# Performance work log

Measured on AMD Instinct MI355X. Metric: run time of the kernel, lower is better.

The kernel has to match this reference:

```python
import jax, jax.numpy as jnp
import numpy as np

MIN_NORM = 1e-15
BALL_EPS = 1e-5  # keep points strictly inside the unit ball (c = 1)


def _artanh(x):
    return jnp.arctanh(jnp.clip(x, -1.0 + BALL_EPS, 1.0 - BALL_EPS))


def expmap0(u):
    # Poincare ball exp map at the origin, c = 1
    n = jnp.clip(jnp.linalg.norm(u, axis=-1, keepdims=True), MIN_NORM)
    return jnp.tanh(n) * u / n


def mobius_matvec(M, x):
    # Mobius matrix-vector product applied to every row of x: [N, D] -> [N, D]
    x_n = jnp.clip(jnp.linalg.norm(x, axis=-1, keepdims=True), MIN_NORM)
    Mx = x @ M.T
    Mx_n = jnp.clip(jnp.linalg.norm(Mx, axis=-1, keepdims=True), MIN_NORM)
    return jnp.tanh(Mx_n / x_n * _artanh(x_n)) * Mx / Mx_n


def pairwise_sqdist(x):
    # sqdist(x_i, x_j) for all pairs via mobius_add(-x_i, x_j); x: [N, D] -> [N, N]
    u = -x[:, None, :]          # [N, 1, D]
    v = x[None, :, :]           # [1, N, D]
    xy = jnp.sum(u * v, axis=-1, keepdims=True)   # [N, N, 1]
    x2 = jnp.sum(u * u, axis=-1, keepdims=True)
    y2 = jnp.sum(v * v, axis=-1, keepdims=True)
    num = (1.0 + 2.0 * xy + y2) * u + (1.0 - x2) * v   # [N, N, D]
    den = jnp.clip(1.0 + 2.0 * xy + x2 * y2, MIN_NORM)
    ma_n = jnp.linalg.norm(num / den, axis=-1)          # [N, N]
    d = 2.0 * _artanh(ma_n)
    return d * d


def setup_inputs() -> dict:
    key = jax.random.key(0)
    k1, k2, k3 = jax.random.split(key, 3)
    N, D, L = 512, 256, 2
    H_euc = jax.random.normal(k1, (N, D), dtype=jnp.float32)
    att_W = jax.random.normal(k2, (L, D, D), dtype=jnp.float32) / np.sqrt(D)
    A = jax.random.randint(k3, (N, N), 0, 2).astype(bool)
    return {"H_euc": H_euc, "att_W": att_W, "A": A}


def reference(H_euc, att_W, A):
    H = expmap0(H_euc)                      # [N, D] on the Poincare ball
    L = att_W.shape[0]
    for l in range(L):
        Wh = mobius_matvec(att_W[l], H)     # one mobius matvec per node (hoisted out of the i,j loop)
        scores = pairwise_sqdist(Wh)        # [N, N] hyperbolic squared distances
        scores = jnp.where(A, scores, -10000.0)
        att = jax.nn.softmax(scores, axis=1)
        att = jnp.where(A, att, 0.0)
        H = att @ H                         # [N, D]
    return H
```

## Files before the change

### kernel.cpp

```cpp
#include <hip/hip_runtime.h>
#include <math.h>

#define NN 512
#define DD 256

__device__ __forceinline__ void wred_sum2(double& a, double& b){
  #pragma unroll
  for (int o = 32; o > 0; o >>= 1){
    a += __shfl_down(a, o);
    b += __shfl_down(b, o);
  }
}
__device__ void bred_sum2(double& a, double& b){
  __shared__ double sa[4], sb[4]; __shared__ double ra, rb;
  int lane = threadIdx.x & 63, w = threadIdx.x >> 6;
  wred_sum2(a, b);
  __syncthreads();
  if (lane == 0){ sa[w] = a; sb[w] = b; }
  __syncthreads();
  if (threadIdx.x == 0){
    ra = (sa[0] + sa[1]) + (sa[2] + sa[3]);
    rb = (sb[0] + sb[1]) + (sb[2] + sb[3]);
  }
  __syncthreads();
  a = ra; b = rb;
}

__device__ __forceinline__ double artanh_clip(double x){
  const double lim = 1.0 - 1e-5;
  if (x >  lim) x =  lim;
  if (x < -lim) x = -lim;
  return 0.5 * log((1.0 + x) / (1.0 - x));
}

__global__ __launch_bounds__(256) void matvec0_k(
    const float* __restrict__ Hin, const float* __restrict__ W,
    const float* __restrict__ W1, float* __restrict__ W1T,
    float* __restrict__ Hf, float* __restrict__ Wh, float* __restrict__ WhT,
    double* __restrict__ r2){
  __shared__ float h0s[DD], h1s[DD];
  __shared__ float tile[64][65];
  int b = blockIdx.x, t = threadIdx.x;
  int i0 = 2 * b, i1 = i0 + 1;
  float u0 = Hin[i0 * DD + t], u1 = Hin[i1 * DD + t];
  double n0 = (double)u0 * (double)u0, n1 = (double)u1 * (double)u1;
  bred_sum2(n0, n1);
  n0 = sqrt(n0); if (n0 < 1e-15) n0 = 1e-15;
  n1 = sqrt(n1); if (n1 < 1e-15) n1 = 1e-15;
  double t0 = tanh(n0), t1 = tanh(n1);
  float h0 = (float)(t0 / n0 * (double)u0);
  float h1 = (float)(t1 / n1 * (double)u1);
  Hf[i0 * DD + t] = h0; Hf[i1 * DD + t] = h1;
  double xn0 = t0 < 1e-15 ? 1e-15 : t0;
  double xn1 = t1 < 1e-15 ? 1e-15 : t1;
  h0s[t] = h0; h1s[t] = h1;
  __syncthreads();
  const float4* Wt = (const float4*)(W + t * DD);
  const float4* r0 = (const float4*)h0s;
  const float4* r1 = (const float4*)h1s;
  float4 A0 = {0,0,0,0}, A1 = {0,0,0,0};
  #pragma unroll 8
  for (int k = 0; k < DD / 4; k++){
    float4 w = Wt[k], x0 = r0[k], x1 = r1[k];
    A0.x = fmaf(x0.x, w.x, A0.x); A0.y = fmaf(x0.y, w.y, A0.y);
    A0.z = fmaf(x0.z, w.z, A0.z); A0.w = fmaf(x0.w, w.w, A0.w);
    A1.x = fmaf(x1.x, w.x, A1.x); A1.y = fmaf(x1.y, w.y, A1.y);
    A1.z = fmaf(x1.z, w.z, A1.z); A1.w = fmaf(x1.w, w.w, A1.w);
  }
  float mx0 = (A0.x + A0.y) + (A0.z + A0.w);
  float mx1 = (A1.x + A1.y) + (A1.z + A1.w);
  double m0 = (double)mx0 * (double)mx0, m1 = (double)mx1 * (double)mx1;
  bred_sum2(m0, m1);
  double mn0 = sqrt(m0); if (mn0 < 1e-15) mn0 = 1e-15;
  double mn1 = sqrt(m1); if (mn1 < 1e-15) mn1 = 1e-15;
  double th0 = tanh(mn0 / xn0 * artanh_clip(xn0));
  double th1 = tanh(mn1 / xn1 * artanh_clip(xn1));
  float w0 = (float)(mx0 * (th0 / mn0));
  float w1 = (float)(mx1 * (th1 / mn1));
  Wh[i0 * DD + t] = w0;  Wh[i1 * DD + t] = w1;
  WhT[t * NN + i0] = w0; WhT[t * NN + i1] = w1;
  if (t == 0){ r2[i0] = th0 * th0; r2[i1] = th1 * th1; }

  if (b < 16){
    int tr = b >> 2, tc = b & 3;
    int tx = t & 63, ty4 = t >> 6;
    #pragma unroll
    for (int yy = 0; yy < 64; yy += 4)
      tile[yy + ty4][tx] = W1[(tr * 64 + yy + ty4) * DD + tc * 64 + tx];
    __syncthreads();
    #pragma unroll
    for (int yy = 0; yy < 64; yy += 4)
      W1T[(tc * 64 + yy + ty4) * DD + tr * 64 + tx] = tile[tx][yy + ty4];
  }
}

template<bool LAST>
__global__ __launch_bounds__(512) void fused_k(
    const float* __restrict__ Wh, const float* __restrict__ WhT,
    const double* __restrict__ r2, const int* __restrict__ A,
    const float* __restrict__ H, const float* __restrict__ WT2,
    float* __restrict__ Hn, float* __restrict__ Whn,
    float* __restrict__ WhTn, double* __restrict__ r2n){
  int b = blockIdx.x, tid = threadIdx.x;
  int i0 = 2 * b;
  __shared__ float xs[2 * DD];
  __shared__ float a_s[2][NN];
  __shared__ float4 parts[1024];
  __shared__ double ssum[8];
  __shared__ float hn_s[2][DD];
  __shared__ double hnorm2[2];

  xs[tid] = Wh[i0 * DD + tid];
  __syncthreads();

  {
    int ks = tid >> 7, jq = tid & 127;
    const float4* WT4 = (const float4*)WhT;
    const float4* x04 = (const float4*)xs;
    const float4* x14 = (const float4*)(xs + DD);
    float4 p0 = {0,0,0,0}, p1 = {0,0,0,0};
    int kq0 = ks * 16;
    #pragma unroll 4
    for (int kk = 0; kk < 16; kk++){
      float4 xa = x04[kq0 + kk], xb = x14[kq0 + kk];
      const float4* wp = WT4 + (kq0 + kk) * 4 * 128 + jq;
      float4 w0 = wp[0], w1 = wp[128], w2 = wp[256], w3 = wp[384];
      p0.x = fmaf(xa.x, w0.x, p0.x); p0.y = fmaf(xa.x, w0.y, p0.y);
      p0.z = fmaf(xa.x, w0.z, p0.z); p0.w = fmaf(xa.x, w0.w, p0.w);
      p0.x = fmaf(xa.y, w1.x, p0.x); p0.y = fmaf(xa.y, w1.y, p0.y);
      p0.z = fmaf(xa.y, w1.z, p0.z); p0.w = fmaf(xa.y, w1.w, p0.w);
      p0.x = fmaf(xa.z, w2.x, p0.x); p0.y = fmaf(xa.z, w2.y, p0.y);
      p0.z = fmaf(xa.z, w2.z, p0.z); p0.w = fmaf(xa.z, w2.w, p0.w);
      p0.x = fmaf(xa.w, w3.x, p0.x); p0.y = fmaf(xa.w, w3.y, p0.y);
      p0.z = fmaf(xa.w, w3.z, p0.z); p0.w = fmaf(xa.w, w3.w, p0.w);
      p1.x = fmaf(xb.x, w0.x, p1.x); p1.y = fmaf(xb.x, w0.y, p1.y);
      p1.z = fmaf(xb.x, w0.z, p1.z); p1.w = fmaf(xb.x, w0.w, p1.w);
      p1.x = fmaf(xb.y, w1.x, p1.x); p1.y = fmaf(xb.y, w1.y, p1.y);
      p1.z = fmaf(xb.y, w1.z, p1.z); p1.w = fmaf(xb.y, w1.w, p1.w);
      p1.x = fmaf(xb.z, w2.x, p1.x); p1.y = fmaf(xb.z, w2.y, p1.y);
      p1.z = fmaf(xb.z, w2.z, p1.z); p1.w = fmaf(xb.z, w2.w, p1.w);
      p1.x = fmaf(xb.w, w3.x, p1.x); p1.y = fmaf(xb.w, w3.y, p1.y);
      p1.z = fmaf(xb.w, w3.z, p1.z); p1.w = fmaf(xb.w, w3.w, p1.w);
    }
    parts[(ks * 128 + jq) * 2 + 0] = p0;
    parts[(ks * 128 + jq) * 2 + 1] = p1;
  }
  __syncthreads();

  int sgC = tid >> 6, qC = tid & 63;
  const float4* H4 = (const float4*)H;
  float4 hpre[8];
  #pragma unroll
  for (int jj = 0; jj < 8; jj++) hpre[jj] = H4[(sgC * 64 + jj) * 64 + qC];

  int r = tid >> 8, j2 = tid & 255;
  int i = i0 + r;
  double X2 = r2[i];
  const float* pf = (const float*)parts;
  auto dsum = [&](int j) -> double {
    int base = (((j >> 2) * 2 + r) << 2) + (j & 3);
    return ((double)pf[base] + (double)pf[base + 1024])
         + ((double)pf[base + 2048] + (double)pf[base + 3072]);
  };
  double d0 = dsum(j2), d1 = dsum(j2 + 256);

  auto score = [&](double dot, double Y2, int jj) -> double {
    if (i == jj) return 0.0;
    double xy = -dot;
    double a  = 1.0 + 2.0 * xy + Y2;
    double bb = 1.0 - X2;
    double den = 1.0 + 2.0 * xy + X2 * Y2;
    if (den < 1e-15) den = 1e-15;
    double nn = a * a * X2 + 2.0 * a * bb * xy + bb * bb * Y2;
    if (nn < 0.0) nn = 0.0;
    double s = sqrt(nn);
    double smax = den * (1.0 - 1e-5);
    if (s > smax) s = smax;
    double d = log((den + s) / (den - s));
    return d * d;
  };

  double Y0 = r2[j2], Y1 = r2[j2 + 256];
  int m0 = A[i * NN + j2], m1 = A[i * NN + j2 + 256];
  double e0 = 0.0, e1 = 0.0;
  if (m0) e0 = exp(score(d0, Y0, j2) - 150.0);
  if (m1) e1 = exp(score(d1, Y1, j2 + 256) - 150.0);

  double part = e0 + e1;
  #pragma unroll
  for (int o = 32; o > 0; o >>= 1) part += __shfl_down(part, o);
  int w = tid >> 6, lane = tid & 63;
  if (lane == 0) ssum[w] = part;
  __syncthreads();
  int base4 = r * 4;
  double sum = (ssum[base4] + ssum[base4 + 1]) + (ssum[base4 + 2] + ssum[base4 + 3]);
  double inv = 1.0 / sum;
  a_s[r][j2]       = m0 ? (float)(e0 * inv) : 0.f;
  a_s[r][j2 + 256] = m1 ? (float)(e1 * inv) : 0.f;
  __syncthreads();

  {
    float4 c0 = {0,0,0,0}, c1 = {0,0,0,0};
    int jb = sgC * 64;
    #pragma unroll
    for (int jj = 0; jj < 8; jj++){
      int j = jb + jj;
      float a0 = a_s[0][j], a1 = a_s[1][j];
      float4 h = hpre[jj];
      c0.x = fmaf(a0, h.x, c0.x); c0.y = fmaf(a0, h.y, c0.y);
      c0.z = fmaf(a0, h.z, c0.z); c0.w = fmaf(a0, h.w, c0.w);
      c1.x = fmaf(a1, h.x, c1.x); c1.y = fmaf(a1, h.y, c1.y);
      c1.z = fmaf(a1, h.z, c1.z); c1.w = fmaf(a1, h.w, c1.w);
    }
    #pragma unroll 8
    for (int jj = 8; jj < 64; jj++){
      int j = jb + jj;
      float a0 = a_s[0][j], a1 = a_s[1][j];
      float4 h = H4[j * 64 + qC];
      c0.x = fmaf(a0, h.x, c0.x); c0.y = fmaf(a0, h.y, c0.y);
      c0.z = fmaf(a0, h.z, c0.z); c0.w = fmaf(a0, h.w, c0.w);
      c1.x = fmaf(a1, h.x, c1.x); c1.y = fmaf(a1, h.y, c1.y);
      c1.z = fmaf(a1, h.z, c1.z); c1.w = fmaf(a1, h.w, c1.w);
    }
    parts[sgC * 64 + qC]       = c0;
    parts[512 + sgC * 64 + qC] = c1;
  }
  __syncthreads();
  if (tid < 128){
    int rr = tid >> 6, qq = tid & 63;
    float4 p[8];
    #pragma unroll
    for (int s8 = 0; s8 < 8; s8++) p[s8] = parts[rr * 512 + s8 * 64 + qq];
    float4 o;
    o.x = ((p[0].x + p[1].x) + (p[2].x + p[3].x)) + ((p[4].x + p[5].x) + (p[6].x + p[7].x));
    o.y = ((p[0].y + p[1].y) + (p[2].y + p[3].y)) + ((p[4].y + p[5].y) + (p[6].y + p[7].y));
    o.z = ((p[0].z + p[1].z) + (p[2].z + p[3].z)) + ((p[4].z + p[5].z) + (p[6].z + p[7].z));
    o.w = ((p[0].w + p[1].w) + (p[2].w + p[3].w)) + ((p[4].w + p[5].w) + (p[6].w + p[7].w));
    ((float4*)(Hn + (i0 + rr) * DD))[qq] = o;
    if (!LAST){
      ((float4*)hn_s[rr])[qq] = o;
      double s = (double)o.x * o.x + (double)o.y * o.y
               + (double)o.z * o.z + (double)o.w * o.w;
      #pragma unroll
      for (int off = 32; off > 0; off >>= 1) s += __shfl_down(s, off);
      if (qq == 0) hnorm2[rr] = s;
    }
  }
  if (LAST) return;
  __syncthreads();

  {
    int ks2 = tid >> 6, dq = tid & 63;
    const float4* WT4b = (const float4*)WT2;
    const float* h0 = hn_s[0]; const float* h1 = hn_s[1];
    float4 p0 = {0,0,0,0}, p1 = {0,0,0,0};
    int k0 = ks2 * 32;
    #pragma unroll 8
    for (int kk = 0; kk < 32; kk++){
      int k = k0 + kk;
      float4 wv = WT4b[k * 64 + dq];
      float a0v = h0[k], a1v = h1[k];
      p0.x = fmaf(a0v, wv.x, p0.x); p0.y = fmaf(a0v, wv.y, p0.y);
      p0.z = fmaf(a0v, wv.z, p0.z); p0.w = fmaf(a0v, wv.w, p0.w);
      p1.x = fmaf(a1v, wv.x, p1.x); p1.y = fmaf(a1v, wv.y, p1.y);
      p1.z = fmaf(a1v, wv.z, p1.z); p1.w = fmaf(a1v, wv.w, p1.w);
    }
    parts[(ks2 * 64 + dq) * 2 + 0] = p0;
    parts[(ks2 * 64 + dq) * 2 + 1] = p1;
  }
  __syncthreads();
  {
    int rr = tid >> 8, d = tid & 255;
    const float* pf2 = (const float*)parts;
    int base = ((d >> 2) * 2 + rr) * 4 + (d & 3);
    float q0 = pf2[base]        + pf2[base + 512];
    float q1 = pf2[base + 1024] + pf2[base + 1536];
    float q2 = pf2[base + 2048] + pf2[base + 2560];
    float q3 = pf2[base + 3072] + pf2[base + 3584];
    float mx = (q0 + q1) + (q2 + q3);
    double m2 = (double)mx * (double)mx;
    #pragma unroll
    for (int o = 32; o > 0; o >>= 1) m2 += __shfl_down(m2, o);
    int w2 = tid >> 6, lane2 = tid & 63;
    if (lane2 == 0) ssum[w2] = m2;
    __syncthreads();
    int b4 = rr * 4;
    double m2sum = (ssum[b4] + ssum[b4 + 1]) + (ssum[b4 + 2] + ssum[b4 + 3]);
    double mn = sqrt(m2sum); if (mn < 1e-15) mn = 1e-15;
    double xn = sqrt(hnorm2[rr]); if (xn < 1e-15) xn = 1e-15;
    double th = tanh(mn / xn * artanh_clip(xn));
    float wv = (float)((double)mx * (th / mn));
    int irow = i0 + rr;
    Whn[irow * DD + d] = wv;
    WhTn[d * NN + irow] = wv;
    if (d == 0) r2n[irow] = th * th;
  }
}

extern "C" void kernel_launch(void* const* d_in, const int* in_sizes, int n_in,
                              void* d_out, int out_size, void* d_ws, size_t ws_size,
                              hipStream_t stream){
  const float* H_euc = (const float*)d_in[0];
  const float* W     = (const float*)d_in[1];
  const int*   A     = (const int*)d_in[2];
  float* out = (float*)d_out;

  float* Hf   = (float*)d_ws;
  float* Hn   = Hf   + NN * DD;
  float* Wh   = Hn   + NN * DD;
  float* WhT  = Wh   + NN * DD;
  float* Whb  = WhT  + NN * DD;
  float* WhTb = Whb  + NN * DD;
  float* W1T  = WhTb + NN * DD;
  double* r2  = (double*)(W1T + DD * DD);
  double* r2b = r2 + NN;

  matvec0_k<<<NN / 2, DD, 0, stream>>>(H_euc, W, W + DD * DD, W1T, Hf, Wh, WhT, r2);
  fused_k<false><<<NN / 2, 2 * DD, 0, stream>>>(Wh, WhT, r2, A, Hf, W1T, Hn, Whb, WhTb, r2b);
  fused_k<true> <<<NN / 2, 2 * DD, 0, stream>>>(Whb, WhTb, r2b, A, Hn, nullptr, out, nullptr, nullptr, nullptr);
}
```

Baseline: 52.92 us.

## Process four rows per block in fused kernel and pre-transpose both weight matrices

The fused attention kernel now handles four query rows per 1024-thread block instead of two. Each loaded WhT, H and W element is reused across four rows, and partial sums are reduced through shared memory in two halves. A separate transpose kernel now produces transposed copies of both layer weights, so the first matvec reads coalesced W0T columns with a split-K reduction instead of strided per-thread rows. The cost is an extra kernel launch, only 128 blocks (fewer than the number of CUs), and higher register and LDS pressure per block.

```diff
diff --git a/kernel.cpp b/kernel.cpp
--- a/kernel.cpp
+++ b/kernel.cpp
@@ -3,6 +3,14 @@
 
 #define NN 512
 #define DD 256
+
+#define FMA4(P, S, V) \
+  P.x = fmaf(S, (V).x, P.x); P.y = fmaf(S, (V).y, P.y); \
+  P.z = fmaf(S, (V).z, P.z); P.w = fmaf(S, (V).w, P.w);
+
+__device__ __forceinline__ float4 f4add(float4 a, float4 b){
+  return make_float4(a.x + b.x, a.y + b.y, a.z + b.z, a.w + b.w);
+}
 
 __device__ __forceinline__ void wred_sum2(double& a, double& b){
   #pragma unroll
@@ -33,15 +41,32 @@
   return 0.5 * log((1.0 + x) / (1.0 - x));
 }
 
+__global__ __launch_bounds__(256) void transpose_k(const float* __restrict__ W,
+                                                   float* __restrict__ W0T,
+                                                   float* __restrict__ W1T){
+  __shared__ float tile[64][65];
+  int b = blockIdx.x, t = threadIdx.x;
+  const float* src = (b < 16) ? W : (W + DD * DD);
+  float* dst = (b < 16) ? W0T : W1T;
+  int tb = b & 15, tr = tb >> 2, tc = tb & 3;
+  int tx = t & 63, ty4 = t >> 6;
+  #pragma unroll
+  for (int yy = 0; yy < 64; yy += 4)
+    tile[yy + ty4][tx] = src[(tr * 64 + yy + ty4) * DD + tc * 64 + tx];
+  __syncthreads();
+  #pragma unroll
+  for (int yy = 0; yy < 64; yy += 4)
+    dst[(tc * 64 + yy + ty4) * DD + tr * 64 + tx] = tile[tx][yy + ty4];
+}
+
 __global__ __launch_bounds__(256) void matvec0_k(
-    const float* __restrict__ Hin, const float* __restrict__ W,
-    const float* __restrict__ W1, float* __restrict__ W1T,
+    const float* __restrict__ Hin, const float* __restrict__ W0T,
     float* __restrict__ Hf, float* __restrict__ Wh, float* __restrict__ WhT,
     double* __restrict__ r2){
-  __shared__ float h0s[DD], h1s[DD];
-  __shared__ float tile[64][65];
   int b = blockIdx.x, t = threadIdx.x;
   int i0 = 2 * b, i1 = i0 + 1;
+  __shared__ float h0s[DD], h1s[DD];
+  __shared__ float4 mp[512];
   float u0 = Hin[i0 * DD + t], u1 = Hin[i1 * DD + t];
   double n0 = (double)u0 * (double)u0, n1 = (double)u1 * (double)u1;
   bred_sum2(n0, n1);
@@ -55,60 +80,55 @@
   double xn1 = t1 < 1e-15 ? 1e-15 : t1;
   h0s[t] = h0; h1s[t] = h1;
   __syncthreads();
-  const float4* Wt = (const float4*)(W + t * DD);
-  const float4* r0 = (const float4*)h0s;
-  const float4* r1 = (const float4*)h1s;
-  float4 A0 = {0,0,0,0}, A1 = {0,0,0,0};
-  #pragma unroll 8
-  for (int k = 0; k < DD / 4; k++){
-    float4 w = Wt[k], x0 = r0[k], x1 = r1[k];
-    A0.x = fmaf(x0.x, w.x, A0.x); A0.y = fmaf(x0.y, w.y, A0.y);
-    A0.z = fmaf(x0.z, w.z, A0.z); A0.w = fmaf(x0.w, w.w, A0.w);
-    A1.x = fmaf(x1.x, w.x, A1.x); A1.y = fmaf(x1.y, w.y, A1.y);
-    A1.z = fmaf(x1.z, w.z, A1.z); A1.w = fmaf(x1.w, w.w, A1.w);
-  }
-  float mx0 = (A0.x + A0.y) + (A0.z + A0.w);
-  float mx1 = (A1.x + A1.y) + (A1.z + A1.w);
+  {
+    int ks = t >> 6, dq = t & 63;
+    const float4* WT4 = (const float4*)W0T;
+    float4 p0 = {0,0,0,0}, p1 = {0,0,0,0};
+    int k0 = ks * 64;
+    #pragma unroll 8
+    for (int kk = 0; kk < 64; kk++){
+      int k = k0 + kk;
+      float4 wv = WT4[k * 64 + dq];
+      float a0 = h0s[k], a1 = h1s[k];
+      FMA4(p0, a0, wv)
+      FMA4(p1, a1, wv)
+    }
+    mp[(ks * 64 + dq) * 2 + 0] = p0;
+    mp[(ks * 64 + dq) * 2 + 1] = p1;
+  }
+  __syncthreads();
+  const float* pf = (const float*)mp;
+  int base = (t >> 2) * 8 + (t & 3);
+  float mx0 = (pf[base]     + pf[base +  512]) + (pf[base + 1024] + pf[base + 1536]);
+  float mx1 = (pf[base + 4] + pf[base +  516]) + (pf[base + 1028] + pf[base + 1540]);
   double m0 = (double)mx0 * (double)mx0, m1 = (double)mx1 * (double)mx1;
   bred_sum2(m0, m1);
   double mn0 = sqrt(m0); if (mn0 < 1e-15) mn0 = 1e-15;
   double mn1 = sqrt(m1); if (mn1 < 1e-15) mn1 = 1e-15;
   double th0 = tanh(mn0 / xn0 * artanh_clip(xn0));
   double th1 = tanh(mn1 / xn1 * artanh_clip(xn1));
-  float w0 = (float)(mx0 * (th0 / mn0));
-  float w1 = (float)(mx1 * (th1 / mn1));
+  float w0 = (float)((double)mx0 * (th0 / mn0));
+  float w1 = (float)((double)mx1 * (th1 / mn1));
   Wh[i0 * DD + t] = w0;  Wh[i1 * DD + t] = w1;
   WhT[t * NN + i0] = w0; WhT[t * NN + i1] = w1;
   if (t == 0){ r2[i0] = th0 * th0; r2[i1] = th1 * th1; }
-
-  if (b < 16){
-    int tr = b >> 2, tc = b & 3;
-    int tx = t & 63, ty4 = t >> 6;
-    #pragma unroll
-    for (int yy = 0; yy < 64; yy += 4)
-      tile[yy + ty4][tx] = W1[(tr * 64 + yy + ty4) * DD + tc * 64 + tx];
-    __syncthreads();
-    #pragma unroll
-    for (int yy = 0; yy < 64; yy += 4)
-      W1T[(tc * 64 + yy + ty4) * DD + tr * 64 + tx] = tile[tx][yy + ty4];
-  }
 }
 
 template<bool LAST>
-__global__ __launch_bounds__(512) void fused_k(
+__global__ __launch_bounds__(1024) void fused_k(
     const float* __restrict__ Wh, const float* __restrict__ WhT,
     const double* __restrict__ r2, const int* __restrict__ A,
     const float* __restrict__ H, const float* __restrict__ WT2,
     float* __restrict__ Hn, float* __restrict__ Whn,
     float* __restrict__ WhTn, double* __restrict__ r2n){
   int b = blockIdx.x, tid = threadIdx.x;
-  int i0 = 2 * b;
-  __shared__ float xs[2 * DD];
-  __shared__ float a_s[2][NN];
-  __shared__ float4 parts[1024];
-  __shared__ double ssum[8];
-  __shared__ float hn_s[2][DD];
-  __shared__ double hnorm2[2];
+  int i0 = 4 * b;
+  __shared__ float xs[4 * DD];
+  __shared__ float a_s[4][NN];
+  __shared__ float4 parts[2048];
+  __shared__ double ssum[16];
+  __shared__ float hn_s[4][DD];
+  __shared__ double hnorm2[4];
 
   xs[tid] = Wh[i0 * DD + tid];
   __syncthreads();
@@ -116,53 +136,53 @@
   {
     int ks = tid >> 7, jq = tid & 127;
     const float4* WT4 = (const float4*)WhT;
-    const float4* x04 = (const float4*)xs;
-    const float4* x14 = (const float4*)(xs + DD);
-    float4 p0 = {0,0,0,0}, p1 = {0,0,0,0};
-    int kq0 = ks * 16;
-    #pragma unroll 4
-    for (int kk = 0; kk < 16; kk++){
-      float4 xa = x04[kq0 + kk], xb = x14[kq0 + kk];
-      const float4* wp = WT4 + (kq0 + kk) * 4 * 128 + jq;
-      float4 w0 = wp[0], w1 = wp[128], w2 = wp[256], w3 = wp[384];
-      p0.x = fmaf(xa.x, w0.x, p0.x); p0.y = fmaf(xa.x, w0.y, p0.y);
-      p0.z = fmaf(xa.x, w0.z, p0.z); p0.w = fmaf(xa.x, w0.w, p0.w);
-      p0.x = fmaf(xa.y, w1.x, p0.x); p0.y = fmaf(xa.y, w1.y, p0.y);
-      p0.z = fmaf(xa.y, w1.z, p0.z); p0.w = fmaf(xa.y, w1.w, p0.w);
-      p0.x = fmaf(xa.z, w2.x, p0.x); p0.y = fmaf(xa.z, w2.y, p0.y);
-      p0.z = fmaf(xa.z, w2.z, p0.z); p0.w = fmaf(xa.z, w2.w, p0.w);
-      p0.x = fmaf(xa.w, w3.x, p0.x); p0.y = fmaf(xa.w, w3.y, p0.y);
-      p0.z = fmaf(xa.w, w3.z, p0.z); p0.w = fmaf(xa.w, w3.w, p0.w);
-      p1.x = fmaf(xb.x, w0.x, p1.x); p1.y = fmaf(xb.x, w0.y, p1.y);
-      p1.z = fmaf(xb.x, w0.z, p1.z); p1.w = fmaf(xb.x, w0.w, p1.w);
-      p1.x = fmaf(xb.y, w1.x, p1.x); p1.y = fmaf(xb.y, w1.y, p1.y);
-      p1.z = fmaf(xb.y, w1.z, p1.z); p1.w = fmaf(xb.y, w1.w, p1.w);
-      p1.x = fmaf(xb.z, w2.x, p1.x); p1.y = fmaf(xb.z, w2.y, p1.y);
-      p1.z = fmaf(xb.z, w2.z, p1.z); p1.w = fmaf(xb.z, w2.w, p1.w);
-      p1.x = fmaf(xb.w, w3.x, p1.x); p1.y = fmaf(xb.w, w3.y, p1.y);
-      p1.z = fmaf(xb.w, w3.z, p1.z); p1.w = fmaf(xb.w, w3.w, p1.w);
-    }
-    parts[(ks * 128 + jq) * 2 + 0] = p0;
-    parts[(ks * 128 + jq) * 2 + 1] = p1;
-  }
-  __syncthreads();
+    const float4* x0 = (const float4*)xs;
+    const float4* x1 = x0 + 64;
+    const float4* x2 = x0 + 128;
+    const float4* x3 = x0 + 192;
+    float4 p0 = {0,0,0,0}, p1 = {0,0,0,0}, p2 = {0,0,0,0}, p3 = {0,0,0,0};
+    int kq0 = ks * 8;
+    #pragma unroll
+    for (int kk = 0; kk < 8; kk++){
+      int kq = kq0 + kk;
+      const float4* wp = WT4 + kq * 512 + jq;
+      float4 wa = wp[0], wb = wp[128], wc = wp[256], wd = wp[384];
+      float4 xa = x0[kq], xb = x1[kq], xc = x2[kq], xd = x3[kq];
+      FMA4(p0, xa.x, wa) FMA4(p0, xa.y, wb) FMA4(p0, xa.z, wc) FMA4(p0, xa.w, wd)
+      FMA4(p1, xb.x, wa) FMA4(p1, xb.y, wb) FMA4(p1, xb.z, wc) FMA4(p1, xb.w, wd)
+      FMA4(p2, xc.x, wa) FMA4(p2, xc.y, wb) FMA4(p2, xc.z, wc) FMA4(p2, xc.w, wd)
+      FMA4(p3, xd.x, wa) FMA4(p3, xd.y, wb) FMA4(p3, xd.z, wc) FMA4(p3, xd.w, wd)
+    }
+    int s4 = ks & 3;
+    int idx = (s4 * 128 + jq) * 4;
+    if (ks >= 4){
+      parts[idx] = p0; parts[idx + 1] = p1; parts[idx + 2] = p2; parts[idx + 3] = p3;
+    }
+    __syncthreads();
+    if (ks < 4){
+      p0 = f4add(p0, parts[idx]);     p1 = f4add(p1, parts[idx + 1]);
+      p2 = f4add(p2, parts[idx + 2]); p3 = f4add(p3, parts[idx + 3]);
+      parts[idx] = p0; parts[idx + 1] = p1; parts[idx + 2] = p2; parts[idx + 3] = p3;
+    }
+    __syncthreads();
+  }
 
   int sgC = tid >> 6, qC = tid & 63;
   const float4* H4 = (const float4*)H;
   float4 hpre[8];
   #pragma unroll
-  for (int jj = 0; jj < 8; jj++) hpre[jj] = H4[(sgC * 64 + jj) * 64 + qC];
-
-  int r = tid >> 8, j2 = tid & 255;
+  for (int jj = 0; jj < 8; jj++) hpre[jj] = H4[(sgC * 32 + jj) * 64 + qC];
+
+  int r = tid >> 8, j = tid & 255;
   int i = i0 + r;
   double X2 = r2[i];
   const float* pf = (const float*)parts;
-  auto dsum = [&](int j) -> double {
-    int base = (((j >> 2) * 2 + r) << 2) + (j & 3);
-    return ((double)pf[base] + (double)pf[base + 1024])
-         + ((double)pf[base + 2048] + (double)pf[base + 3072]);
-  };
-  double d0 = dsum(j2), d1 = dsum(j2 + 256);
+  int basep = (j >> 2) * 16 + r * 4 + (j & 3);
+  double d0 = ((double)pf[basep]        + (double)pf[basep + 2048])
+            + ((double)pf[basep + 4096] + (double)pf[basep + 6144]);
+  int basep2 = basep + 1024;
+  double d1 = ((double)pf[basep2]        + (double)pf[basep2 + 2048])
+            + ((double)pf[basep2 + 4096] + (double)pf[basep2 + 6144]);
 
   auto score = [&](double dot, double Y2, int jj) -> double {
     if (i == jj) return 0.0;
@@ -180,11 +200,11 @@
     return d * d;
   };
 
-  double Y0 = r2[j2], Y1 = r2[j2 + 256];
-  int m0 = A[i * NN + j2], m1 = A[i * NN + j2 + 256];
+  double Y0 = r2[j], Y1 = r2[j + 256];
+  int m0 = A[i * NN + j], m1 = A[i * NN + j + 256];
   double e0 = 0.0, e1 = 0.0;
-  if (m0) e0 = exp(score(d0, Y0, j2) - 150.0);
-  if (m1) e1 = exp(score(d1, Y1, j2 + 256) - 150.0);
+  if (m0) e0 = exp(score(d0, Y0, j) - 150.0);
+  if (m1) e1 = exp(score(d1, Y1, j + 256) - 150.0);
 
   double part = e0 + e1;
   #pragma unroll
@@ -192,100 +212,100 @@
   int w = tid >> 6, lane = tid & 63;
   if (lane == 0) ssum[w] = part;
   __syncthreads();
-  int base4 = r * 4;
-  double sum = (ssum[base4] + ssum[base4 + 1]) + (ssum[base4 + 2] + ssum[base4 + 3]);
+  int b4 = r * 4;
+  double sum = (ssum[b4] + ssum[b4 + 1]) + (ssum[b4 + 2] + ssum[b4 + 3]);
   double inv = 1.0 / sum;
-  a_s[r][j2]       = m0 ? (float)(e0 * inv) : 0.f;
-  a_s[r][j2 + 256] = m1 ? (float)(e1 * inv) : 0.f;
-  __syncthreads();
-
-  {
-    float4 c0 = {0,0,0,0}, c1 = {0,0,0,0};
-    int jb = sgC * 64;
+  a_s[r][j]       = m0 ? (float)(e0 * inv) : 0.f;
+  a_s[r][j + 256] = m1 ? (float)(e1 * inv) : 0.f;
+  __syncthreads();
+
+  {
+    float4 c0 = {0,0,0,0}, c1 = {0,0,0,0}, c2 = {0,0,0,0}, c3 = {0,0,0,0};
+    int jb = sgC * 32;
     #pragma unroll
     for (int jj = 0; jj < 8; jj++){
-      int j = jb + jj;
-      float a0 = a_s[0][j], a1 = a_s[1][j];
+      int jx = jb + jj;
+      float a0 = a_s[0][jx], a1 = a_s[1][jx], a2 = a_s[2][jx], a3 = a_s[3][jx];
       float4 h = hpre[jj];
-      c0.x = fmaf(a0, h.x, c0.x); c0.y = fmaf(a0, h.y, c0.y);
-      c0.z = fmaf(a0, h.z, c0.z); c0.w = fmaf(a0, h.w, c0.w);
-      c1.x = fmaf(a1, h.x, c1.x); c1.y = fmaf(a1, h.y, c1.y);
-      c1.z = fmaf(a1, h.z, c1.z); c1.w = fmaf(a1, h.w, c1.w);
+      FMA4(c0, a0, h) FMA4(c1, a1, h) FMA4(c2, a2, h) FMA4(c3, a3, h)
     }
     #pragma unroll 8
-    for (int jj = 8; jj < 64; jj++){
-      int j = jb + jj;
-      float a0 = a_s[0][j], a1 = a_s[1][j];
-      float4 h = H4[j * 64 + qC];
-      c0.x = fmaf(a0, h.x, c0.x); c0.y = fmaf(a0, h.y, c0.y);
-      c0.z = fmaf(a0, h.z, c0.z); c0.w = fmaf(a0, h.w, c0.w);
-      c1.x = fmaf(a1, h.x, c1.x); c1.y = fmaf(a1, h.y, c1.y);
-      c1.z = fmaf(a1, h.z, c1.z); c1.w = fmaf(a1, h.w, c1.w);
-    }
-    parts[sgC * 64 + qC]       = c0;
-    parts[512 + sgC * 64 + qC] = c1;
-  }
-  __syncthreads();
-  if (tid < 128){
+    for (int jj = 8; jj < 32; jj++){
+      int jx = jb + jj;
+      float4 h = H4[jx * 64 + qC];
+      float a0 = a_s[0][jx], a1 = a_s[1][jx], a2 = a_s[2][jx], a3 = a_s[3][jx];
+      FMA4(c0, a0, h) FMA4(c1, a1, h) FMA4(c2, a2, h) FMA4(c3, a3, h)
+    }
+    int s8 = sgC & 7;
+    int idx = (s8 * 64 + qC) * 4;
+    if (sgC >= 8){
+      parts[idx] = c0; parts[idx + 1] = c1; parts[idx + 2] = c2; parts[idx + 3] = c3;
+    }
+    __syncthreads();
+    if (sgC < 8){
+      c0 = f4add(c0, parts[idx]);     c1 = f4add(c1, parts[idx + 1]);
+      c2 = f4add(c2, parts[idx + 2]); c3 = f4add(c3, parts[idx + 3]);
+      parts[idx] = c0; parts[idx + 1] = c1; parts[idx + 2] = c2; parts[idx + 3] = c3;
+    }
+    __syncthreads();
+  }
+  if (tid < 256){
     int rr = tid >> 6, qq = tid & 63;
-    float4 p[8];
+    float4 o = {0,0,0,0};
     #pragma unroll
-    for (int s8 = 0; s8 < 8; s8++) p[s8] = parts[rr * 512 + s8 * 64 + qq];
-    float4 o;
-    o.x = ((p[0].x + p[1].x) + (p[2].x + p[3].x)) + ((p[4].x + p[5].x) + (p[6].x + p[7].x));
-    o.y = ((p[0].y + p[1].y) + (p[2].y + p[3].y)) + ((p[4].y + p[5].y) + (p[6].y + p[7].y));
-    o.z = ((p[0].z + p[1].z) + (p[2].z + p[3].z)) + ((p[4].z + p[5].z) + (p[6].z + p[7].z));
-    o.w = ((p[0].w + p[1].w) + (p[2].w + p[3].w)) + ((p[4].w + p[5].w) + (p[6].w + p[7].w));
+    for (int s = 0; s < 8; s++) o = f4add(o, parts[(s * 64 + qq) * 4 + rr]);
     ((float4*)(Hn + (i0 + rr) * DD))[qq] = o;
     if (!LAST){
       ((float4*)hn_s[rr])[qq] = o;
-      double s = (double)o.x * o.x + (double)o.y * o.y
-               + (double)o.z * o.z + (double)o.w * o.w;
+      double s2 = (double)o.x * o.x + (double)o.y * o.y
+                + (double)o.z * o.z + (double)o.w * o.w;
       #pragma unroll
-      for (int off = 32; off > 0; off >>= 1) s += __shfl_down(s, off);
-      if (qq == 0) hnorm2[rr] = s;
+      for (int off = 32; off > 0; off >>= 1) s2 += __shfl_down(s2, off);
+      if (qq == 0) hnorm2[rr] = s2;
     }
   }
   if (LAST) return;
   __syncthreads();
 
   {
-    int ks2 = tid >> 6, dq = tid & 63;
+    int ks = tid >> 6, dq = tid & 63;
     const float4* WT4b = (const float4*)WT2;
-    const float* h0 = hn_s[0]; const float* h1 = hn_s[1];
-    float4 p0 = {0,0,0,0}, p1 = {0,0,0,0};
-    int k0 = ks2 * 32;
+    float4 p0 = {0,0,0,0}, p1 = {0,0,0,0}, p2 = {0,0,0,0}, p3 = {0,0,0,0};
+    int k0 = ks * 16;
     #pragma unroll 8
-    for (int kk = 0; kk < 32; kk++){
+    for (int kk = 0; kk < 16; kk++){
       int k = k0 + kk;
       float4 wv = WT4b[k * 64 + dq];
-      float a0v = h0[k], a1v = h1[k];
-      p0.x = fmaf(a0v, wv.x, p0.x); p0.y = fmaf(a0v, wv.y, p0.y);
-      p0.z = fmaf(a0v, wv.z, p0.z); p0.w = fmaf(a0v, wv.w, p0.w);
-      p1.x = fmaf(a1v, wv.x, p1.x); p1.y = fmaf(a1v, wv.y, p1.y);
-      p1.z = fmaf(a1v, wv.z, p1.z); p1.w = fmaf(a1v, wv.w, p1.w);
-    }
-    parts[(ks2 * 64 + dq) * 2 + 0] = p0;
-    parts[(ks2 * 64 + dq) * 2 + 1] = p1;
-  }
-  __syncthreads();
+      float a0 = hn_s[0][k], a1 = hn_s[1][k], a2 = hn_s[2][k], a3 = hn_s[3][k];
+      FMA4(p0, a0, wv) FMA4(p1, a1, wv) FMA4(p2, a2, wv) FMA4(p3, a3, wv)
+    }
+    int s8 = ks & 7;
+    int idx = (s8 * 64 + dq) * 4;
+    if (ks >= 8){
+      parts[idx] = p0; parts[idx + 1] = p1; parts[idx + 2] = p2; parts[idx + 3] = p3;
+    }
+    __syncthreads();
+    if (ks < 8){
+      p0 = f4add(p0, parts[idx]);     p1 = f4add(p1, parts[idx + 1]);
+      p2 = f4add(p2, parts[idx + 2]); p3 = f4add(p3, parts[idx + 3]);
+      parts[idx] = p0; parts[idx + 1] = p1; parts[idx + 2] = p2; parts[idx + 3] = p3;
+    }
+    __syncthreads();
+  }
   {
     int rr = tid >> 8, d = tid & 255;
     const float* pf2 = (const float*)parts;
-    int base = ((d >> 2) * 2 + rr) * 4 + (d & 3);
-    float q0 = pf2[base]        + pf2[base + 512];
-    float q1 = pf2[base + 1024] + pf2[base + 1536];
-    float q2 = pf2[base + 2048] + pf2[base + 2560];
-    float q3 = pf2[base + 3072] + pf2[base + 3584];
-    float mx = (q0 + q1) + (q2 + q3);
+    int bb = (d >> 2) * 16 + rr * 4 + (d & 3);
+    float mx = ((pf2[bb]        + pf2[bb + 1024]) + (pf2[bb + 2048] + pf2[bb + 3072]))
+             + ((pf2[bb + 4096] + pf2[bb + 5120]) + (pf2[bb + 6144] + pf2[bb + 7168]));
     double m2 = (double)mx * (double)mx;
     #pragma unroll
     for (int o = 32; o > 0; o >>= 1) m2 += __shfl_down(m2, o);
     int w2 = tid >> 6, lane2 = tid & 63;
     if (lane2 == 0) ssum[w2] = m2;
     __syncthreads();
-    int b4 = rr * 4;
-    double m2sum = (ssum[b4] + ssum[b4 + 1]) + (ssum[b4 + 2] + ssum[b4 + 3]);
+    int b42 = rr * 4;
+    double m2sum = (ssum[b42] + ssum[b42 + 1]) + (ssum[b42 + 2] + ssum[b42 + 3]);
     double mn = sqrt(m2sum); if (mn < 1e-15) mn = 1e-15;
     double xn = sqrt(hnorm2[rr]); if (xn < 1e-15) xn = 1e-15;
     double th = tanh(mn / xn * artanh_clip(xn));
@@ -311,11 +331,13 @@
   float* WhT  = Wh   + NN * DD;
   float* Whb  = WhT  + NN * DD;
   float* WhTb = Whb  + NN * DD;
-  float* W1T  = WhTb + NN * DD;
+  float* W0T  = WhTb + NN * DD;
+  float* W1T  = W0T  + DD * DD;
   double* r2  = (double*)(W1T + DD * DD);
   double* r2b = r2 + NN;
 
-  matvec0_k<<<NN / 2, DD, 0, stream>>>(H_euc, W, W + DD * DD, W1T, Hf, Wh, WhT, r2);
-  fused_k<false><<<NN / 2, 2 * DD, 0, stream>>>(Wh, WhT, r2, A, Hf, W1T, Hn, Whb, WhTb, r2b);
-  fused_k<true> <<<NN / 2, 2 * DD, 0, stream>>>(Whb, WhTb, r2b, A, Hn, nullptr, out, nullptr, nullptr, nullptr);
-}
+  transpose_k<<<32, 256, 0, stream>>>(W, W0T, W1T);
+  matvec0_k<<<NN / 2, 256, 0, stream>>>(H_euc, W0T, Hf, Wh, WhT, r2);
+  fused_k<false><<<NN / 4, 1024, 0, stream>>>(Wh, WhT, r2, A, Hf, W1T, Hn, Whb, WhTb, r2b);
+  fused_k<true> <<<NN / 4, 1024, 0, stream>>>(Whb, WhTb, r2b, A, Hn, nullptr, out, nullptr, nullptr, nullptr);
+}
```

Result: slower. 73.47 us (+38.8%).

## Transpose both weight matrices in a separate kernel and coalesce the layer-0 matvec

Applied to the files above, without the earlier changes.

Moves the W1 transpose out of matvec0_k into a new transpose kernel that also transposes W0. The layer-0 matvec then reads W0T coalesced (threads span output columns, split-K over 4 warps, reduced through shared memory) instead of each thread striding a full row of W. fused_k also prefetches more H rows (16 instead of 8) and the first 8 W1T rows before the softmax phase, to hide global-load latency. The cost is an extra kernel launch, more registers in fused_k, and an extra shared-memory reduction in matvec0_k.

```diff
diff --git a/kernel.cpp b/kernel.cpp
--- a/kernel.cpp
+++ b/kernel.cpp
@@ -3,6 +3,14 @@
 
 #define NN 512
 #define DD 256
+
+#define FMA4(P, S, V) \
+  P.x = fmaf(S, (V).x, P.x); P.y = fmaf(S, (V).y, P.y); \
+  P.z = fmaf(S, (V).z, P.z); P.w = fmaf(S, (V).w, P.w);
+
+__device__ __forceinline__ float4 f4add(float4 a, float4 b){
+  return make_float4(a.x + b.x, a.y + b.y, a.z + b.z, a.w + b.w);
+}
 
 __device__ __forceinline__ void wred_sum2(double& a, double& b){
   #pragma unroll
@@ -33,15 +41,32 @@
   return 0.5 * log((1.0 + x) / (1.0 - x));
 }
 
+__global__ __launch_bounds__(256) void transpose_k(const float* __restrict__ W,
+                                                   float* __restrict__ W0T,
+                                                   float* __restrict__ W1T){
+  __shared__ float tile[64][65];
+  int b = blockIdx.x, t = threadIdx.x;
+  const float* src = (b < 16) ? W : (W + DD * DD);
+  float* dst = (b < 16) ? W0T : W1T;
+  int tb = b & 15, tr = tb >> 2, tc = tb & 3;
+  int tx = t & 63, ty4 = t >> 6;
+  #pragma unroll
+  for (int yy = 0; yy < 64; yy += 4)
+    tile[yy + ty4][tx] = src[(tr * 64 + yy + ty4) * DD + tc * 64 + tx];
+  __syncthreads();
+  #pragma unroll
+  for (int yy = 0; yy < 64; yy += 4)
+    dst[(tc * 64 + yy + ty4) * DD + tr * 64 + tx] = tile[tx][yy + ty4];
+}
+
 __global__ __launch_bounds__(256) void matvec0_k(
-    const float* __restrict__ Hin, const float* __restrict__ W,
-    const float* __restrict__ W1, float* __restrict__ W1T,
+    const float* __restrict__ Hin, const float* __restrict__ W0T,
     float* __restrict__ Hf, float* __restrict__ Wh, float* __restrict__ WhT,
     double* __restrict__ r2){
-  __shared__ float h0s[DD], h1s[DD];
-  __shared__ float tile[64][65];
   int b = blockIdx.x, t = threadIdx.x;
   int i0 = 2 * b, i1 = i0 + 1;
+  __shared__ float h0s[DD], h1s[DD];
+  __shared__ float4 mp[512];
   float u0 = Hin[i0 * DD + t], u1 = Hin[i1 * DD + t];
   double n0 = (double)u0 * (double)u0, n1 = (double)u1 * (double)u1;
   bred_sum2(n0, n1);
@@ -55,43 +80,38 @@
   double xn1 = t1 < 1e-15 ? 1e-15 : t1;
   h0s[t] = h0; h1s[t] = h1;
   __syncthreads();
-  const float4* Wt = (const float4*)(W + t * DD);
-  const float4* r0 = (const float4*)h0s;
-  const float4* r1 = (const float4*)h1s;
-  float4 A0 = {0,0,0,0}, A1 = {0,0,0,0};
-  #pragma unroll 8
-  for (int k = 0; k < DD / 4; k++){
-    float4 w = Wt[k], x0 = r0[k], x1 = r1[k];
-    A0.x = fmaf(x0.x, w.x, A0.x); A0.y = fmaf(x0.y, w.y, A0.y);
-    A0.z = fmaf(x0.z, w.z, A0.z); A0.w = fmaf(x0.w, w.w, A0.w);
-    A1.x = fmaf(x1.x, w.x, A1.x); A1.y = fmaf(x1.y, w.y, A1.y);
-    A1.z = fmaf(x1.z, w.z, A1.z); A1.w = fmaf(x1.w, w.w, A1.w);
-  }
-  float mx0 = (A0.x + A0.y) + (A0.z + A0.w);
-  float mx1 = (A1.x + A1.y) + (A1.z + A1.w);
+  {
+    int ks = t >> 6, dq = t & 63;
+    const float4* WT4 = (const float4*)W0T;
+    float4 p0 = {0,0,0,0}, p1 = {0,0,0,0};
+    int k0 = ks * 64;
+    #pragma unroll 8
+    for (int kk = 0; kk < 64; kk++){
+      int k = k0 + kk;
+      float4 wv = WT4[k * 64 + dq];
+      float a0 = h0s[k], a1 = h1s[k];
+      FMA4(p0, a0, wv)
+      FMA4(p1, a1, wv)
+    }
+    mp[(ks * 64 + dq) * 2 + 0] = p0;
+    mp[(ks * 64 + dq) * 2 + 1] = p1;
+  }
+  __syncthreads();
+  const float* pf = (const float*)mp;
+  int base = (t >> 2) * 8 + (t & 3);
+  float mx0 = (pf[base]     + pf[base +  512]) + (pf[base + 1024] + pf[base + 1536]);
+  float mx1 = (pf[base + 4] + pf[base +  516]) + (pf[base + 1028] + pf[base + 1540]);
   double m0 = (double)mx0 * (double)mx0, m1 = (double)mx1 * (double)mx1;
   bred_sum2(m0, m1);
   double mn0 = sqrt(m0); if (mn0 < 1e-15) mn0 = 1e-15;
   double mn1 = sqrt(m1); if (mn1 < 1e-15) mn1 = 1e-15;
   double th0 = tanh(mn0 / xn0 * artanh_clip(xn0));
   double th1 = tanh(mn1 / xn1 * artanh_clip(xn1));
-  float w0 = (float)(mx0 * (th0 / mn0));
-  float w1 = (float)(mx1 * (th1 / mn1));
+  float w0 = (float)((double)mx0 * (th0 / mn0));
+  float w1 = (float)((double)mx1 * (th1 / mn1));
   Wh[i0 * DD + t] = w0;  Wh[i1 * DD + t] = w1;
   WhT[t * NN + i0] = w0; WhT[t * NN + i1] = w1;
   if (t == 0){ r2[i0] = th0 * th0; r2[i1] = th1 * th1; }
-
-  if (b < 16){
-    int tr = b >> 2, tc = b & 3;
-    int tx = t & 63, ty4 = t >> 6;
-    #pragma unroll
-    for (int yy = 0; yy < 64; yy += 4)
-      tile[yy + ty4][tx] = W1[(tr * 64 + yy + ty4) * DD + tc * 64 + tx];
-    __syncthreads();
-    #pragma unroll
-    for (int yy = 0; yy < 64; yy += 4)
-      W1T[(tc * 64 + yy + ty4) * DD + tr * 64 + tx] = tile[tx][yy + ty4];
-  }
 }
 
 template<bool LAST>
@@ -124,23 +144,9 @@
     for (int kk = 0; kk < 16; kk++){
       float4 xa = x04[kq0 + kk], xb = x14[kq0 + kk];
       const float4* wp = WT4 + (kq0 + kk) * 4 * 128 + jq;
-      float4 w0 = wp[0], w1 = wp[128], w2 = wp[256], w3 = wp[384];
-      p0.x = fmaf(xa.x, w0.x, p0.x); p0.y = fmaf(xa.x, w0.y, p0.y);
-      p0.z = fmaf(xa.x, w0.z, p0.z); p0.w = fmaf(xa.x, w0.w, p0.w);
-      p0.x = fmaf(xa.y, w1.x, p0.x); p0.y = fmaf(xa.y, w1.y, p0.y);
-      p0.z = fmaf(xa.y, w1.z, p0.z); p0.w = fmaf(xa.y, w1.w, p0.w);
-      p0.x = fmaf(xa.z, w2.x, p0.x); p0.y = fmaf(xa.z, w2.y, p0.y);
-      p0.z = fmaf(xa.z, w2.z, p0.z); p0.w = fmaf(xa.z, w2.w, p0.w);
-      p0.x = fmaf(xa.w, w3.x, p0.x); p0.y = fmaf(xa.w, w3.y, p0.y);
-      p0.z = fmaf(xa.w, w3.z, p0.z); p0.w = fmaf(xa.w, w3.w, p0.w);
-      p1.x = fmaf(xb.x, w0.x, p1.x); p1.y = fmaf(xb.x, w0.y, p1.y);
-      p1.z = fmaf(xb.x, w0.z, p1.z); p1.w = fmaf(xb.x, w0.w, p1.w);
-      p1.x = fmaf(xb.y, w1.x, p1.x); p1.y = fmaf(xb.y, w1.y, p1.y);
-      p1.z = fmaf(xb.y, w1.z, p1.z); p1.w = fmaf(xb.y, w1.w, p1.w);
-      p1.x = fmaf(xb.z, w2.x, p1.x); p1.y = fmaf(xb.z, w2.y, p1.y);
-      p1.z = fmaf(xb.z, w2.z, p1.z); p1.w = fmaf(xb.z, w2.w, p1.w);
-      p1.x = fmaf(xb.w, w3.x, p1.x); p1.y = fmaf(xb.w, w3.y, p1.y);
-      p1.z = fmaf(xb.w, w3.z, p1.z); p1.w = fmaf(xb.w, w3.w, p1.w);
+      float4 wa = wp[0], wb = wp[128], wc = wp[256], wd = wp[384];
+      FMA4(p0, xa.x, wa) FMA4(p0, xa.y, wb) FMA4(p0, xa.z, wc) FMA4(p0, xa.w, wd)
+      FMA4(p1, xb.x, wa) FMA4(p1, xb.y, wb) FMA4(p1, xb.z, wc) FMA4(p1, xb.w, wd)
     }
     parts[(ks * 128 + jq) * 2 + 0] = p0;
     parts[(ks * 128 + jq) * 2 + 1] = p1;
@@ -149,9 +155,16 @@
 
   int sgC = tid >> 6, qC = tid & 63;
   const float4* H4 = (const float4*)H;
-  float4 hpre[8];
-  #pragma unroll
-  for (int jj = 0; jj < 8; jj++) hpre[jj] = H4[(sgC * 64 + jj) * 64 + qC];
+  float4 hpre[16];
+  #pragma unroll
+  for (int jj = 0; jj < 16; jj++) hpre[jj] = H4[(sgC * 64 + jj) * 64 + qC];
+  float4 wpre[8];
+  if (!LAST){
+    const float4* WT4b = (const float4*)WT2;
+    int k0w = sgC * 32;
+    #pragma unroll
+    for (int kk = 0; kk < 8; kk++) wpre[kk] = WT4b[(k0w + kk) * 64 + qC];
+  }
 
   int r = tid >> 8, j2 = tid & 255;
   int i = i0 + r;
@@ -203,24 +216,18 @@
     float4 c0 = {0,0,0,0}, c1 = {0,0,0,0};
     int jb = sgC * 64;
     #pragma unroll
-    for (int jj = 0; jj < 8; jj++){
+    for (int jj = 0; jj < 16; jj++){
       int j = jb + jj;
       float a0 = a_s[0][j], a1 = a_s[1][j];
       float4 h = hpre[jj];
-      c0.x = fmaf(a0, h.x, c0.x); c0.y = fmaf(a0, h.y, c0.y);
-      c0.z = fmaf(a0, h.z, c0.z); c0.w = fmaf(a0, h.w, c0.w);
-      c1.x = fmaf(a1, h.x, c1.x); c1.y = fmaf(a1, h.y, c1.y);
-      c1.z = fmaf(a1, h.z, c1.z); c1.w = fmaf(a1, h.w, c1.w);
+      FMA4(c0, a0, h) FMA4(c1, a1, h)
     }
     #pragma unroll 8
-    for (int jj = 8; jj < 64; jj++){
+    for (int jj = 16; jj < 64; jj++){
       int j = jb + jj;
       float a0 = a_s[0][j], a1 = a_s[1][j];
       float4 h = H4[j * 64 + qC];
-      c0.x = fmaf(a0, h.x, c0.x); c0.y = fmaf(a0, h.y, c0.y);
-      c0.z = fmaf(a0, h.z, c0.z); c0.w = fmaf(a0, h.w, c0.w);
-      c1.x = fmaf(a1, h.x, c1.x); c1.y = fmaf(a1, h.y, c1.y);
-      c1.z = fmaf(a1, h.z, c1.z); c1.w = fmaf(a1, h.w, c1.w);
+      FMA4(c0, a0, h) FMA4(c1, a1, h)
     }
     parts[sgC * 64 + qC]       = c0;
     parts[512 + sgC * 64 + qC] = c1;
@@ -250,20 +257,24 @@
   __syncthreads();
 
   {
-    int ks2 = tid >> 6, dq = tid & 63;
+    int ks2 = sgC, dq = qC;
     const float4* WT4b = (const float4*)WT2;
     const float* h0 = hn_s[0]; const float* h1 = hn_s[1];
     float4 p0 = {0,0,0,0}, p1 = {0,0,0,0};
     int k0 = ks2 * 32;
+    #pragma unroll
+    for (int kk = 0; kk < 8; kk++){
+      int k = k0 + kk;
+      float4 wv = wpre[kk];
+      float a0v = h0[k], a1v = h1[k];
+      FMA4(p0, a0v, wv) FMA4(p1, a1v, wv)
+    }
     #pragma unroll 8
-    for (int kk = 0; kk < 32; kk++){
+    for (int kk = 8; kk < 32; kk++){
       int k = k0 + kk;
       float4 wv = WT4b[k * 64 + dq];
       float a0v = h0[k], a1v = h1[k];
-      p0.x = fmaf(a0v, wv.x, p0.x); p0.y = fmaf(a0v, wv.y, p0.y);
-      p0.z = fmaf(a0v, wv.z, p0.z); p0.w = fmaf(a0v, wv.w, p0.w);
-      p1.x = fmaf(a1v, wv.x, p1.x); p1.y = fmaf(a1v, wv.y, p1.y);
-      p1.z = fmaf(a1v, wv.z, p1.z); p1.w = fmaf(a1v, wv.w, p1.w);
+      FMA4(p0, a0v, wv) FMA4(p1, a1v, wv)
     }
     parts[(ks2 * 64 + dq) * 2 + 0] = p0;
     parts[(ks2 * 64 + dq) * 2 + 1] = p1;
@@ -311,11 +322,13 @@
   float* WhT  = Wh   + NN * DD;
   float* Whb  = WhT  + NN * DD;
   float* WhTb = Whb  + NN * DD;
-  float* W1T  = WhTb + NN * DD;
+  float* W0T  = WhTb + NN * DD;
+  float* W1T  = W0T  + DD * DD;
   double* r2  = (double*)(W1T + DD * DD);
   double* r2b = r2 + NN;
 
-  matvec0_k<<<NN / 2, DD, 0, stream>>>(H_euc, W, W + DD * DD, W1T, Hf, Wh, WhT, r2);
+  transpose_k<<<32, 256, 0, stream>>>(W, W0T, W1T);
+  matvec0_k<<<NN / 2, 256, 0, stream>>>(H_euc, W0T, Hf, Wh, WhT, r2);
   fused_k<false><<<NN / 2, 2 * DD, 0, stream>>>(Wh, WhT, r2, A, Hf, W1T, Hn, Whb, WhTb, r2b);
   fused_k<true> <<<NN / 2, 2 * DD, 0, stream>>>(Whb, WhTb, r2b, A, Hn, nullptr, out, nullptr, nullptr, nullptr);
 }
```

New measurement: 64.18 us. +21.3%, slower.
